# Performance work log

Measured on AMD Instinct MI355X. Metric: run time of the kernel, lower is better.

## Reference

```python
import jax, jax.numpy as jnp
import numpy as np

ITERS = 3

def squash(x, axis=-1):
    norm = jnp.linalg.norm(x, axis=axis, keepdims=True)
    scale = norm ** 2 / (1 + norm ** 2) / (norm + 1e-08)
    return scale * x

def setup_inputs() -> dict:
    key = jax.random.key(0)
    kx, kw = jax.random.split(key)
    x = jax.random.normal(kx, (64, 8000, 8), dtype=jnp.float32)
    W = 0.01 * jax.random.normal(kw, (10, 8000, 16, 8), dtype=jnp.float32)
    return {"x": x, "W": W}

def reference(x, W):
    # u_hat[b,o,i,d] = W[o,i,d,e] @ x[b,i,e]
    u_hat = jnp.einsum('oide,bie->boid', W, x)  # [B, O, I, D]
    temp_u_hat = jax.lax.stop_gradient(u_hat)
    B, O, I, D = u_hat.shape
    b = jnp.zeros((B, O, I, 1), dtype=u_hat.dtype)
    v = jnp.ones((B, O, D), dtype=u_hat.dtype)
    for i in range(ITERS):
        c = jax.nn.softmax(b, axis=1)  # over out_caps
        if i < ITERS - 1:
            s = (c * temp_u_hat).sum(axis=2)       # [B, O, D]
            v = squash(s)
            # agreement: u_hat . v over dim D
            b = b + jnp.einsum('boid,bod->boi', temp_u_hat, v)[..., None]
        else:
            s = (c * u_hat).sum(axis=2)
            v = squash(s)
    return v
```

## Files before the change

### kernel.cpp

```cpp
#include <hip/hip_runtime.h>
#include <hip/hip_fp16.h>
#include <math.h>

#define IN 8000
#define OC 10
#define NSTAGE 500
#define VACC_F (64 * OC * 16)
#define PART_H (64 * OC * 16)

typedef __fp16 h2 __attribute__((ext_vector_type(2)));
typedef _Float16 half8 __attribute__((ext_vector_type(8)));
typedef float f32x16 __attribute__((ext_vector_type(16)));

__device__ __forceinline__ h2 asb(unsigned int v) { return __builtin_bit_cast(h2, v); }

__device__ __forceinline__ float dot2(h2 a, h2 b, float c) {
#if __has_builtin(__builtin_amdgcn_fdot2)
    return __builtin_amdgcn_fdot2(a, b, c, false);
#else
    return fmaf((float)a[0], (float)b[0], fmaf((float)a[1], (float)b[1], c));
#endif
}

__device__ __forceinline__ unsigned int pk_rn(float a, float b) {
    return __builtin_bit_cast(unsigned int, __float22half2_rn(make_float2(a, b)));
}

#define WL_OFF 0
#define XL_OFF 40960
#define ZS_OFF 57600
#define SM_BYTES 57616

template<int UNIFORM>
__global__ __launch_bounds__(256, 2) void caps_pass(
    const float* __restrict__ W, const float* __restrict__ x,
    const float* __restrict__ Vacc, __fp16* __restrict__ part)
{
    __shared__ __align__(16) unsigned char sm[SM_BYTES];
    unsigned short* Wl = (unsigned short*)(sm + WL_OFF);
    unsigned short* xl = (unsigned short*)(sm + XL_OFF);

    const int t    = threadIdx.x;
    const int w    = t >> 6;
    const int lane = t & 63;
    const int lo   = lane & 31;
    const int hi   = lane >> 5;
    const int bt   = w & 1;
    const int ph   = w >> 1;
    const int b    = bt * 32 + lo;

    if (t < 4) ((unsigned int*)(sm + ZS_OFF))[t] = 0u;

    h2 vh[10][4];
    if (!UNIFORM) {
        const float* vp = Vacc + (size_t)b * (OC * 16);
        const float L2E = 1.44269504f;
#pragma unroll
        for (int o = 0; o < OC; ++o) {
            float4 fa = *(const float4*)(vp + o * 16 + 4 * hi);
            float4 fb = *(const float4*)(vp + o * 16 + 8 + 4 * hi);
            vh[o][0] = asb(pk_rn(fa.x * L2E, fa.y * L2E));
            vh[o][1] = asb(pk_rn(fa.z * L2E, fa.w * L2E));
            vh[o][2] = asb(pk_rn(fb.x * L2E, fb.y * L2E));
            vh[o][3] = asb(pk_rn(fb.z * L2E, fb.w * L2E));
        }
    }

    f32x16 acc[5];
#pragma unroll
    for (int op = 0; op < 5; ++op)
#pragma unroll
        for (int k = 0; k < 16; ++k) acc[op][k] = 0.f;

    f32x16 zc;
#pragma unroll
    for (int k = 0; k < 16; ++k) zc[k] = 0.f;

    const int bid  = blockIdx.x;
    const int grid = gridDim.x;

    for (int st = bid; st < NSTAGE; st += grid) {
        const int is = st * 16;
        __syncthreads();
        for (int j = t; j < 5120; j += 256) {
            int il  = j / 320;
            int rem = j - il * 320;
            int o   = rem >> 5;
            int r   = rem & 31;
            float4 w4 = *(const float4*)(W + (size_t)o * (IN * 128) +
                                         (size_t)(is + il) * 128 + r * 4);
            *(uint2*)&Wl[il * 1280 + o * 128 + r * 4] =
                make_uint2(pk_rn(w4.x, w4.y), pk_rn(w4.z, w4.w));
        }
        for (int j = t; j < 2048; j += 256) {
            int bb = j >> 5;
            int r  = j & 31;
            int il = r >> 1;
            int hh = r & 1;
            float4 x4 = *(const float4*)(x + (size_t)bb * (IN * 8) +
                                         (size_t)(is + il) * 8 + hh * 4);
            *(uint2*)&xl[il * 520 + bb * 8 + hh * 4] =
                make_uint2(pk_rn(x4.x, x4.y), pk_rn(x4.z, x4.w));
        }
        __syncthreads();

        if (UNIFORM) {
#pragma unroll
            for (int ip = 0; ip < 4; ++ip) {
                const int il0 = (ph * 4 + ip) * 2;
                half8 xb = *(const half8*)(sm + XL_OFF + (il0 + hi) * 1040 + b * 16);
#pragma unroll
                for (int op = 0; op < 5; ++op) {
                    half8 av = *(const half8*)(sm + WL_OFF + (il0 + hi) * 2560 +
                                               op * 512 + lo * 16);
                    acc[op] = __builtin_amdgcn_mfma_f32_32x32x16_f16(av, xb, acc[op], 0, 0, 0);
                }
            }
        } else {
#pragma unroll 1
            for (int u = 0; u < 8; ++u) {
                const int il = ph * 8 + u;
                const unsigned char* xaddr = (lane < 32)
                    ? (sm + XL_OFF + il * 1040 + b * 16)
                    : (sm + ZS_OFF);
                half8 xb = *(const half8*)xaddr;

                h2 uh2[5][8];
                float lgf[10];
#pragma unroll
                for (int op = 0; op < 5; ++op) {
                    half8 av = *(const half8*)(sm + WL_OFF + il * 2560 +
                                               op * 512 + lo * 16);
                    f32x16 C = __builtin_amdgcn_mfma_f32_32x32x16_f16(av, xb, zc, 0, 0, 0);
#pragma unroll
                    for (int q = 0; q < 8; ++q)
                        uh2[op][q] = __builtin_amdgcn_cvt_pkrtz(C[2 * q], C[2 * q + 1]);
                    float l0 = 0.f, l1 = 0.f;
#pragma unroll
                    for (int qq = 0; qq < 4; ++qq) {
                        l0 = dot2(uh2[op][qq],     vh[op * 2][qq],     l0);
                        l1 = dot2(uh2[op][4 + qq], vh[op * 2 + 1][qq], l1);
                    }
                    lgf[op * 2]     = l0;
                    lgf[op * 2 + 1] = l1;
                }
#pragma unroll
                for (int pp = 0; pp < 5; ++pp) {
                    h2 lp = asb(pk_rn(lgf[2 * pp], lgf[2 * pp + 1]));
                    int ob = __shfl_xor(__builtin_bit_cast(int, lp), 32);
                    h2 s2 = lp + __builtin_bit_cast(h2, ob);
                    lgf[2 * pp]     = (float)s2[0];
                    lgf[2 * pp + 1] = (float)s2[1];
                }
                float mx = lgf[0];
#pragma unroll
                for (int o = 1; o < OC; ++o) mx = fmaxf(mx, lgf[o]);
                float pe[10];
                float se = 0.f;
#pragma unroll
                for (int o = 0; o < OC; ++o) {
                    pe[o] = __builtin_amdgcn_exp2f(lgf[o] - mx);
                    se += pe[o];
                }
                float rs = __builtin_amdgcn_rcpf(se);
                float c10[10];
#pragma unroll
                for (int o = 0; o < OC; ++o) c10[o] = pe[o] * rs;
#pragma unroll
                for (int op = 0; op < 5; ++op)
#pragma unroll
                    for (int r = 0; r < 16; ++r) {
                        float uv = (float)uh2[op][r >> 1][r & 1];
                        acc[op][r] = fmaf(c10[op * 2 + (r >> 3)], uv, acc[op][r]);
                    }
            }
        }
    }

    float* red = (float*)sm;
#pragma unroll 1
    for (int phase = 0; phase < 2; ++phase) {
        __syncthreads();
        if (ph == phase) {
#pragma unroll
            for (int op = 0; op < 5; ++op)
#pragma unroll
                for (int rp = 0; rp < 8; ++rp) {
                    const int r = rp * 2;
                    const int o = op * 2 + (r >> 3);
                    const int d = (r & 3) + 8 * ((r >> 2) & 1) + 4 * hi;
                    float* p = &red[(size_t)b * 164 + o * 16 + d];
                    if (phase == 0) {
                        *(float2*)p = make_float2(acc[op][r], acc[op][r + 1]);
                    } else {
                        float2 v2 = *(const float2*)p;
                        v2.x += acc[op][r];
                        v2.y += acc[op][r + 1];
                        *(float2*)p = v2;
                    }
                }
        }
    }
    __syncthreads();
    unsigned int* dst = (unsigned int*)part;
    for (int q = t; q < PART_H / 2; q += 256) {
        int bo = q >> 3;
        int u8 = q & 7;
        int bb = bo / 10;
        int oo = bo - bb * 10;
        float2 v2 = *(const float2*)&red[(size_t)bb * 164 + oo * 16 + u8 * 2];
        dst[(size_t)(bo * grid + bid) * 8 + u8] = pk_rn(v2.x, v2.y);
    }
}

__global__ __launch_bounds__(256) void caps_reduce(
    const __fp16* __restrict__ part, float* __restrict__ Vacc,
    float* __restrict__ out, int nchunk, int mode, float scale)
{
    const int bo = blockIdx.x;
    const int t  = threadIdx.x;
    const int d2 = t & 3;
    const int s  = t >> 2;

    const unsigned int* p32 = (const unsigned int*)part + (size_t)bo * nchunk * 8;
    float4 a = make_float4(0.f, 0.f, 0.f, 0.f);
    for (int c = s; c < nchunk; c += 64) {
        uint2 v = *(const uint2*)(p32 + (size_t)c * 8 + d2 * 2);
        h2 lov = asb(v.x), hiv = asb(v.y);
        a.x += (float)lov[0]; a.y += (float)lov[1];
        a.z += (float)hiv[0]; a.w += (float)hiv[1];
    }
#pragma unroll
    for (int m = 4; m <= 32; m <<= 1) {
        a.x += __shfl_xor(a.x, m); a.y += __shfl_xor(a.y, m);
        a.z += __shfl_xor(a.z, m); a.w += __shfl_xor(a.w, m);
    }
    __shared__ float red[4][16];
    const int wv = t >> 6;
    if ((t & 63) < 4) {
        red[wv][d2 * 4 + 0] = a.x; red[wv][d2 * 4 + 1] = a.y;
        red[wv][d2 * 4 + 2] = a.z; red[wv][d2 * 4 + 3] = a.w;
    }
    __syncthreads();
    if (t < 16) {
        float sv = (red[0][t] + red[1][t] + red[2][t] + red[3][t]) * scale;
        float n2 = sv * sv;
#pragma unroll
        for (int m = 1; m < 16; m <<= 1) n2 += __shfl_xor(n2, m);
        float norm = sqrtf(n2);
        float scl  = n2 / (1.f + n2) / (norm + 1e-8f);
        float v = scl * sv;
        if (mode == 2)      out[bo * 16 + t] = v;
        else if (mode == 0) Vacc[bo * 16 + t] = v;
        else                Vacc[bo * 16 + t] += v;
    }
}

extern "C" void kernel_launch(void* const* d_in, const int* in_sizes, int n_in,
                              void* d_out, int out_size, void* d_ws, size_t ws_size,
                              hipStream_t stream) {
    const float* x = (const float*)d_in[0];
    const float* W = (const float*)d_in[1];
    float* out = (float*)d_out;

    char* ws = (char*)d_ws;
    float*  Vacc = (float*)ws;
    __fp16* part = (__fp16*)(ws + VACC_F * sizeof(float));

    size_t avail = (ws_size > VACC_F * sizeof(float)) ? ws_size - VACC_F * sizeof(float) : 0;
    long slots = (long)(avail / (PART_H * sizeof(__fp16)));
    int grid = (int)((slots < NSTAGE) ? slots : NSTAGE);
    if (grid < 1) grid = 1;

    caps_pass<1><<<grid, 256, 0, stream>>>(W, x, Vacc, part);
    caps_reduce<<<640, 256, 0, stream>>>(part, Vacc, out, grid, 0, 0.1f);
    caps_pass<0><<<grid, 256, 0, stream>>>(W, x, Vacc, part);
    caps_reduce<<<640, 256, 0, stream>>>(part, Vacc, out, grid, 1, 1.0f);
    caps_pass<0><<<grid, 256, 0, stream>>>(W, x, Vacc, part);
    caps_reduce<<<640, 256, 0, stream>>>(part, Vacc, out, grid, 2, 1.0f);
}
```

Measured before the change: 182.7 us.

## Pre-pack W and x to fp16 records, double-buffer via global_load_lds

Adds a prep kernel that converts W and x once into fp16 per-unit records laid out to match the shared-memory tiles. The three routing passes then stream these half-size records straight into LDS with asynchronous global-to-LDS loads, double-buffered over units of 8 input capsules. This removes the repeated fp32 reads and conversions in every pass and overlaps loading with MFMA work. In exchange it adds an extra kernel launch, a workspace buffer of about 28 MB, and extra barriers per unit.

```diff
diff --git a/kernel.cpp b/kernel.cpp
--- a/kernel.cpp
+++ b/kernel.cpp
@@ -4,9 +4,15 @@
 
 #define IN 8000
 #define OC 10
-#define NSTAGE 500
+#define NUNIT 1000
 #define VACC_F (64 * OC * 16)
 #define PART_H (64 * OC * 16)
+
+#define REC_B   28672
+#define REC_H   14336
+#define XOFF_B  20480
+#define XOFF_H  10240
+#define REC_TOTAL_B ((size_t)NUNIT * REC_B)
 
 typedef __fp16 h2 __attribute__((ext_vector_type(2)));
 typedef _Float16 half8 __attribute__((ext_vector_type(8)));
@@ -26,19 +32,56 @@
     return __builtin_bit_cast(unsigned int, __float22half2_rn(make_float2(a, b)));
 }
 
-#define WL_OFF 0
-#define XL_OFF 40960
-#define ZS_OFF 57600
-#define SM_BYTES 57616
+#define GLDS16(gp, lp) __builtin_amdgcn_global_load_lds(                      \
+    (const __attribute__((address_space(1))) void*)(gp),                      \
+    (__attribute__((address_space(3))) void*)(lp), 16, 0, 0)
+
+__global__ __launch_bounds__(256) void caps_prep(
+    const float* __restrict__ W, const float* __restrict__ x,
+    __fp16* __restrict__ rec)
+{
+    const int t   = threadIdx.x;
+    const int blk = blockIdx.x;
+    if (blk < 1250) {
+        const int gt = blk * 256 + t;
+#pragma unroll
+        for (int k = 0; k < 4; ++k) {
+            int g  = gt + k * 320000;
+            int u  = g / 1280;
+            int r  = g - u * 1280;
+            int il = r / 160;
+            int rr = r - il * 160;
+            int o  = rr >> 4;
+            int d  = rr & 15;
+            const float* ip = W + ((size_t)o * IN + (size_t)(u * 8 + il)) * 128 + d * 8;
+            float4 f0 = *(const float4*)(ip);
+            float4 f1 = *(const float4*)(ip + 4);
+            uint4 pk = make_uint4(pk_rn(f0.x, f0.y), pk_rn(f0.z, f0.w),
+                                  pk_rn(f1.x, f1.y), pk_rn(f1.z, f1.w));
+            *(uint4*)(rec + (size_t)u * REC_H + il * 1280 + o * 128 + d * 8) = pk;
+        }
+    } else {
+        const int u    = (blk - 1250) * 4 + (t >> 6);
+        const int lane = t & 63;
+#pragma unroll
+        for (int il = 0; il < 8; ++il) {
+            const float* ip = x + ((size_t)lane * IN + (size_t)(u * 8 + il)) * 8;
+            float4 f0 = *(const float4*)(ip);
+            float4 f1 = *(const float4*)(ip + 4);
+            uint4 pk = make_uint4(pk_rn(f0.x, f0.y), pk_rn(f0.z, f0.w),
+                                  pk_rn(f1.x, f1.y), pk_rn(f1.z, f1.w));
+            *(uint4*)(rec + (size_t)u * REC_H + XOFF_H + il * 512 + lane * 8) = pk;
+        }
+    }
+}
 
 template<int UNIFORM>
 __global__ __launch_bounds__(256, 2) void caps_pass(
-    const float* __restrict__ W, const float* __restrict__ x,
-    const float* __restrict__ Vacc, __fp16* __restrict__ part)
+    const __fp16* __restrict__ rec, const float* __restrict__ Vacc,
+    __fp16* __restrict__ part)
 {
-    __shared__ __align__(16) unsigned char sm[SM_BYTES];
-    unsigned short* Wl = (unsigned short*)(sm + WL_OFF);
-    unsigned short* xl = (unsigned short*)(sm + XL_OFF);
+    __shared__ __align__(16) unsigned char sm[2 * REC_B];
+    __shared__ __align__(16) unsigned char zs[16];
 
     const int t    = threadIdx.x;
     const int w    = t >> 6;
@@ -49,7 +92,7 @@
     const int ph   = w >> 1;
     const int b    = bt * 32 + lo;
 
-    if (t < 4) ((unsigned int*)(sm + ZS_OFF))[t] = 0u;
+    if (t < 4) ((unsigned int*)zs)[t] = 0u;
 
     h2 vh[10][4];
     if (!UNIFORM) {
@@ -79,58 +122,49 @@
     const int bid  = blockIdx.x;
     const int grid = gridDim.x;
 
-    for (int st = bid; st < NSTAGE; st += grid) {
-        const int is = st * 16;
-        __syncthreads();
-        for (int j = t; j < 5120; j += 256) {
-            int il  = j / 320;
-            int rem = j - il * 320;
-            int o   = rem >> 5;
-            int r   = rem & 31;
-            float4 w4 = *(const float4*)(W + (size_t)o * (IN * 128) +
-                                         (size_t)(is + il) * 128 + r * 4);
-            *(uint2*)&Wl[il * 1280 + o * 128 + r * 4] =
-                make_uint2(pk_rn(w4.x, w4.y), pk_rn(w4.z, w4.w));
-        }
-        for (int j = t; j < 2048; j += 256) {
-            int bb = j >> 5;
-            int r  = j & 31;
-            int il = r >> 1;
-            int hh = r & 1;
-            float4 x4 = *(const float4*)(x + (size_t)bb * (IN * 8) +
-                                         (size_t)(is + il) * 8 + hh * 4);
-            *(uint2*)&xl[il * 520 + bb * 8 + hh * 4] =
-                make_uint2(pk_rn(x4.x, x4.y), pk_rn(x4.z, x4.w));
-        }
-        __syncthreads();
+    auto issue = [&](int st, int bufi) {
+        const char* g = (const char*)rec + (size_t)st * REC_B + (size_t)lane * 16;
+        unsigned char* lb = sm + bufi * REC_B;
+#pragma unroll
+        for (int c = 0; c < 7; ++c) {
+            const int q = c * 4 + w;
+            GLDS16(g + q * 1024, lb + q * 1024);
+        }
+    };
+
+    issue(bid, 0);
+    if (bid + grid < NUNIT) issue(bid + grid, 1);
+    __syncthreads();
+
+    int cur = 0;
+    for (int st = bid; st < NUNIT; st += grid) {
+        const unsigned char* buf = sm + cur * REC_B;
 
         if (UNIFORM) {
 #pragma unroll
-            for (int ip = 0; ip < 4; ++ip) {
-                const int il0 = (ph * 4 + ip) * 2;
-                half8 xb = *(const half8*)(sm + XL_OFF + (il0 + hi) * 1040 + b * 16);
+            for (int ip = 0; ip < 2; ++ip) {
+                const int il0 = ph * 4 + ip * 2;
+                half8 xb = *(const half8*)(buf + XOFF_B + (il0 + hi) * 1024 + b * 16);
 #pragma unroll
                 for (int op = 0; op < 5; ++op) {
-                    half8 av = *(const half8*)(sm + WL_OFF + (il0 + hi) * 2560 +
-                                               op * 512 + lo * 16);
+                    half8 av = *(const half8*)(buf + (il0 + hi) * 2560 + op * 512 + lo * 16);
                     acc[op] = __builtin_amdgcn_mfma_f32_32x32x16_f16(av, xb, acc[op], 0, 0, 0);
                 }
             }
         } else {
 #pragma unroll 1
-            for (int u = 0; u < 8; ++u) {
-                const int il = ph * 8 + u;
+            for (int u = 0; u < 4; ++u) {
+                const int il = ph * 4 + u;
                 const unsigned char* xaddr = (lane < 32)
-                    ? (sm + XL_OFF + il * 1040 + b * 16)
-                    : (sm + ZS_OFF);
+                    ? (buf + XOFF_B + il * 1024 + b * 16)
+                    : (const unsigned char*)zs;
                 half8 xb = *(const half8*)xaddr;
 
                 h2 uh2[5][8];
                 float lgf[10];
 #pragma unroll
                 for (int op = 0; op < 5; ++op) {
-                    half8 av = *(const half8*)(sm + WL_OFF + il * 2560 +
-                                               op * 512 + lo * 16);
+                    half8 av = *(const half8*)(buf + il * 2560 + op * 512 + lo * 16);
                     f32x16 C = __builtin_amdgcn_mfma_f32_32x32x16_f16(av, xb, zc, 0, 0, 0);
 #pragma unroll
                     for (int q = 0; q < 8; ++q)
@@ -175,6 +209,14 @@
                     }
             }
         }
+
+        const int nxt = st + 2 * grid;
+        if (nxt < NUNIT) {
+            __syncthreads();
+            issue(nxt, cur);
+            __syncthreads();
+        }
+        cur ^= 1;
     }
 
     float* red = (float*)sm;
@@ -265,17 +307,21 @@
 
     char* ws = (char*)d_ws;
     float*  Vacc = (float*)ws;
-    __fp16* part = (__fp16*)(ws + VACC_F * sizeof(float));
-
-    size_t avail = (ws_size > VACC_F * sizeof(float)) ? ws_size - VACC_F * sizeof(float) : 0;
+    __fp16* rec  = (__fp16*)(ws + VACC_F * sizeof(float));
+    __fp16* part = (__fp16*)(ws + VACC_F * sizeof(float) + REC_TOTAL_B);
+
+    size_t head = VACC_F * sizeof(float) + REC_TOTAL_B;
+    size_t avail = (ws_size > head) ? ws_size - head : 0;
     long slots = (long)(avail / (PART_H * sizeof(__fp16)));
-    int grid = (int)((slots < NSTAGE) ? slots : NSTAGE);
+    int grid = (int)((slots < 500) ? slots : 500);
     if (grid < 1) grid = 1;
 
-    caps_pass<1><<<grid, 256, 0, stream>>>(W, x, Vacc, part);
+    caps_prep<<<1500, 256, 0, stream>>>(W, x, rec);
+
+    caps_pass<1><<<grid, 256, 0, stream>>>(rec, Vacc, part);
     caps_reduce<<<640, 256, 0, stream>>>(part, Vacc, out, grid, 0, 0.1f);
-    caps_pass<0><<<grid, 256, 0, stream>>>(W, x, Vacc, part);
+    caps_pass<0><<<grid, 256, 0, stream>>>(rec, Vacc, part);
     caps_reduce<<<640, 256, 0, stream>>>(part, Vacc, out, grid, 1, 1.0f);
-    caps_pass<0><<<grid, 256, 0, stream>>>(W, x, Vacc, part);
+    caps_pass<0><<<grid, 256, 0, stream>>>(rec, Vacc, part);
     caps_reduce<<<640, 256, 0, stream>>>(part, Vacc, out, grid, 2, 1.0f);
 }
```

Result: faster. 166.6 us (-8.8%).
